# Optimization experiments

Measured on AMD Instinct MI355X. Metric: run time of the kernel, lower is better.

Reference implementation:

```python
import jax, jax.numpy as jnp
import numpy as np

N_NODES = 100000
N_EDGES = 3200000
D_FEAT = 512


def setup_inputs() -> dict:
    key = jax.random.key(0)
    k1, k2, k3, k4 = jax.random.split(key, 4)
    x = jax.random.normal(k1, (N_NODES, D_FEAT), dtype=jnp.float32)
    edge_index = jax.random.randint(k2, (2, N_EDGES), 0, N_NODES, dtype=jnp.int64)
    # Glorot-ish init for GCN layer weights
    W1 = jax.random.normal(k3, (D_FEAT, 16), dtype=jnp.float32) * (1.0 / np.sqrt(D_FEAT))
    b1 = jnp.zeros((16,), dtype=jnp.float32)
    W2 = jax.random.normal(k4, (16, 2), dtype=jnp.float32) * (1.0 / np.sqrt(16))
    b2 = jnp.zeros((2,), dtype=jnp.float32)
    return {"x": x, "edge_index": edge_index, "W1": W1, "b1": b1, "W2": W2, "b2": b2}


def _gcn_prep(edge_index, n_nodes):
    # add self-loops and compute symmetric normalization (GCNConv default)
    row = jnp.concatenate([edge_index[0], jnp.arange(n_nodes, dtype=edge_index.dtype)])
    col = jnp.concatenate([edge_index[1], jnp.arange(n_nodes, dtype=edge_index.dtype)])
    deg = jax.ops.segment_sum(jnp.ones_like(row, dtype=jnp.float32), row,
                              num_segments=n_nodes)
    deg_isqrt = jnp.where(deg > 0, jax.lax.rsqrt(deg), 0.0)
    norm = deg_isqrt[row] * deg_isqrt[col]  # [E+N]
    return row, col, norm


def _gcn_conv(x, W, b, row, col, norm, n_nodes):
    h = x @ W                              # [N, out]
    msg = h[col] * norm[:, None]           # gather + scale  [E+N, out]
    out = jax.ops.segment_sum(msg, row, num_segments=n_nodes)  # scatter-add
    return out + b


def reference(x, edge_index, W1, b1, W2, b2):
    n_nodes = x.shape[0]
    row, col, norm = _gcn_prep(edge_index, n_nodes)
    h = _gcn_conv(x, W1, b1, row, col, norm, n_nodes)
    h = jax.nn.relu(h)
    # dropout is identity in eval mode (deterministic reference)
    h = _gcn_conv(h, W2, b2, row, col, norm, n_nodes)
    return jax.nn.log_softmax(h, axis=1)
```

## Files before the change

### kernel.cpp

```cpp
#include <hip/hip_runtime.h>
#include <math.h>


#define DF 512
#define H1F 16
#define BROWS 256
#define PA_VPT 16
#define PA_BATCH 4096
#define A2_CAP 10240

typedef short bf16x8 __attribute__((ext_vector_type(8)));
typedef float f32x4 __attribute__((ext_vector_type(4)));
typedef _Float16 half8 __attribute__((ext_vector_type(8)));

static __device__ __forceinline__ short bf16_rne(float f) {
    unsigned int u = __builtin_bit_cast(unsigned int, f);
    unsigned int r = (u + 0x7FFFu + ((u >> 16) & 1u)) >> 16;
    return (short)r;
}

__global__ __launch_bounds__(256) void k_hist(const int* __restrict__ rowi,
                                              unsigned int* __restrict__ ghist,
                                              int E, int nbkt, int nblkp) {
    __shared__ unsigned int hist[512];
    int t = threadIdx.x;
    hist[t] = 0u; hist[t + 256] = 0u;
    __syncthreads();
    int base = blockIdx.x * PA_BATCH;
    int ne = E - base; if (ne > PA_BATCH) ne = PA_BATCH;
    for (int j = t; j < ne; j += 256)
        atomicAdd(&hist[(unsigned int)rowi[base + j] >> 8], 1u);
    __syncthreads();
    for (int b = t; b < nbkt; b += 256)
        ghist[(size_t)b * nblkp + blockIdx.x] = hist[b];
}

__global__ __launch_bounds__(256) void k_colscan(const unsigned int* __restrict__ ghist,
                                                 unsigned int* __restrict__ gbase,
                                                 unsigned int* __restrict__ btot,
                                                 int nblk, int nblkp) {
    __shared__ unsigned int s[256];
    int t = threadIdx.x, b = blockIdx.x;
    unsigned int carry = 0u;
    int nch = (nblk + 255) / 256;
    for (int ch = 0; ch < nch; ++ch) {
        int idx = ch * 256 + t;
        unsigned int v = (idx < nblk) ? ghist[(size_t)b * nblkp + idx] : 0u;
        s[t] = v;
        __syncthreads();
        for (int off = 1; off < 256; off <<= 1) {
            unsigned int u = (t >= off) ? s[t - off] : 0u;
            __syncthreads();
            s[t] += u;
            __syncthreads();
        }
        if (idx < nblk) gbase[(size_t)b * nblkp + idx] = carry + s[t] - v;
        unsigned int tot = s[255];
        __syncthreads();
        carry += tot;
    }
    if (t == 0) btot[b] = carry;
}

__global__ __launch_bounds__(256) void k_scatter(const int* __restrict__ rowi,
                                                 const int* __restrict__ coli,
                                                 const unsigned int* __restrict__ gbase,
                                                 const unsigned int* __restrict__ btot,
                                                 unsigned int* __restrict__ pairs,
                                                 int E, int nbkt, int nblkp) {
    __shared__ unsigned int hist[512];
    __shared__ unsigned int sA[512];
    __shared__ unsigned int sB[512];
    __shared__ unsigned int gb[512];
    __shared__ unsigned int reorder[PA_BATCH];
    __shared__ unsigned short bid[PA_BATCH];
    int t = threadIdx.x;
    int base = blockIdx.x * PA_BATCH;
    int ne = E - base; if (ne > PA_BATCH) ne = PA_BATCH;

    unsigned int b0 = (t < nbkt) ? btot[t] : 0u;
    unsigned int b1v = (t + 256 < nbkt) ? btot[t + 256] : 0u;
    sA[t] = b0; sA[t + 256] = b1v;
    __syncthreads();
    {
        unsigned int* src = sA; unsigned int* dst = sB;
        for (int off = 1; off < 512; off <<= 1) {
            unsigned int v0 = src[t] + ((t >= off) ? src[t - off] : 0u);
            unsigned int v1 = src[t + 256] + src[t + 256 - off];
            dst[t] = v0; dst[t + 256] = v1;
            __syncthreads();
            unsigned int* tmp = src; src = dst; dst = tmp;
        }
        gb[t] = src[t] - b0;
        gb[t + 256] = src[t + 256] - b1v;
        if (t < nbkt) gb[t] += gbase[(size_t)t * nblkp + blockIdx.x];
        if (t + 256 < nbkt) gb[t + 256] += gbase[(size_t)(t + 256) * nblkp + blockIdx.x];
    }

    hist[t] = 0u; hist[t + 256] = 0u;
    __syncthreads();

    unsigned int pk[PA_VPT]; unsigned int bk[PA_VPT]; unsigned int rk[PA_VPT];
#pragma unroll
    for (int j = 0; j < PA_VPT; ++j) {
        int idx = j * 256 + t;
        if (idx < ne) {
            int r = rowi[base + idx];
            int c = coli[base + idx];
            unsigned int b = (unsigned int)r >> 8;
            pk[j] = ((unsigned int)(r & (BROWS - 1)) << 17) | (unsigned int)c;
            bk[j] = b;
            rk[j] = atomicAdd(&hist[b], 1u);
        } else bk[j] = 0xFFFFFFFFu;
    }
    __syncthreads();

    sA[t] = hist[t]; sA[t + 256] = hist[t + 256];
    __syncthreads();
    unsigned int* src = sA; unsigned int* dst = sB;
    for (int off = 1; off < 512; off <<= 1) {
        unsigned int v0 = src[t] + ((t >= off) ? src[t - off] : 0u);
        unsigned int v1 = src[t + 256] + src[t + 256 - off];
        dst[t] = v0; dst[t + 256] = v1;
        __syncthreads();
        unsigned int* tmp = src; src = dst; dst = tmp;
    }

#pragma unroll
    for (int j = 0; j < PA_VPT; ++j) {
        if (bk[j] != 0xFFFFFFFFu) {
            unsigned int b = bk[j];
            unsigned int slot = src[b] - hist[b] + rk[j];
            reorder[slot] = pk[j];
            bid[slot] = (unsigned short)b;
        }
    }
    __syncthreads();

    for (int s = t; s < ne; s += 256) {
        unsigned int b = bid[s];
        unsigned int off = src[b] - hist[b];
        pairs[gb[b] + ((unsigned int)s - off)] = reorder[s];
    }
}

__global__ __launch_bounds__(512) void k_count(const unsigned int* __restrict__ pairs,
                                               const unsigned int* __restrict__ btot,
                                               unsigned int* __restrict__ bpref_g,
                                               unsigned int* __restrict__ deg,
                                               unsigned int* __restrict__ rowloc,
                                               float* __restrict__ isq, int n, int nbkt) {
    __shared__ unsigned int bsc[512];
    __shared__ unsigned int rcnt[256];
    __shared__ unsigned int ssc[256];
    int t = threadIdx.x;
    int b = blockIdx.x;
    int r0 = b * 256;

    bsc[t] = (t < nbkt) ? btot[t] : 0u;
    __syncthreads();
    for (int off = 1; off < 512; off <<= 1) {
        unsigned int u = (t >= off) ? bsc[t - off] : 0u;
        __syncthreads();
        bsc[t] += u;
        __syncthreads();
    }
    unsigned int bp = (b > 0) ? bsc[b - 1] : 0u;
    unsigned int cnt = btot[b];
    if (t == 0) bpref_g[b] = bp;
    if (cnt > A2_CAP) cnt = A2_CAP;

    if (t < 256) rcnt[t] = 0u;
    __syncthreads();
    for (unsigned int i = t; i < cnt; i += 512)
        atomicAdd(&rcnt[pairs[bp + i] >> 17], 1u);
    __syncthreads();
    unsigned int d = 0;
    if (t < 256) { d = rcnt[t]; ssc[t] = d; }
    __syncthreads();
    for (int off = 1; off < 256; off <<= 1) {
        unsigned int u = 0;
        if (t < 256 && t >= off) u = ssc[t - off];
        __syncthreads();
        if (t < 256) ssc[t] += u;
        __syncthreads();
    }
    if (t < 256 && r0 + t < n) {
        deg[r0 + t] = d;
        rowloc[r0 + t] = ssc[t] - d;
        isq[r0 + t] = rsqrtf((float)(d + 1u));
    }
}

__global__ __launch_bounds__(256) void k_gemm1(const float* __restrict__ x,
                                               const float* __restrict__ W1,
                                               const float* __restrict__ isq,
                                               _Float16* __restrict__ h1h,
                                               int n, int ntile, int tstride) {
    int wave = threadIdx.x >> 6;
    int lane = threadIdx.x & 63;
    int g = lane >> 4;
    int m = lane & 15;

    bf16x8 wf[16];
#pragma unroll
    for (int s = 0; s < 16; ++s) {
#pragma unroll
        for (int j = 0; j < 8; ++j) {
            int k = s * 32 + g * 8 + j;
            wf[s][j] = bf16_rne(W1[k * H1F + m]);
        }
    }

    for (int tile = blockIdx.x * 4 + wave; tile < ntile; tile += tstride) {
        long r0 = (long)tile * 16;
        const float* xrow = x + (r0 + m) * DF;
        f32x4 acc = {0.0f, 0.0f, 0.0f, 0.0f};
#pragma unroll
        for (int s = 0; s < 16; ++s) {
            const float4* p = (const float4*)(xrow + s * 32 + g * 8);
            float4 a0 = p[0];
            float4 a1 = p[1];
            bf16x8 af;
            af[0] = bf16_rne(a0.x); af[1] = bf16_rne(a0.y);
            af[2] = bf16_rne(a0.z); af[3] = bf16_rne(a0.w);
            af[4] = bf16_rne(a1.x); af[5] = bf16_rne(a1.y);
            af[6] = bf16_rne(a1.z); af[7] = bf16_rne(a1.w);
            acc = __builtin_amdgcn_mfma_f32_16x16x32_bf16(af, wf[s], acc, 0, 0, 0);
        }
#pragma unroll
        for (int j = 0; j < 4; ++j) {
            long rr = r0 + g * 4 + j;
            h1h[rr * H1F + m] = (_Float16)(isq[rr] * acc[j]);
        }
    }
}

__global__ __launch_bounds__(1024) void k_sortg1(unsigned int* __restrict__ pairs,
                                                 const unsigned int* __restrict__ btot,
                                                 const unsigned int* __restrict__ bpref_g,
                                                 const unsigned int* __restrict__ rowloc,
                                                 const float* __restrict__ isq,
                                                 const _Float16* __restrict__ h1h,
                                                 const float* __restrict__ b1,
                                                 _Float16* __restrict__ r1h, int n) {
    __shared__ unsigned int sorted[A2_CAP];
    __shared__ unsigned int rloc[256];
    __shared__ unsigned int rcur[256];
    int t = threadIdx.x;
    int b = blockIdx.x;
    int r0 = b * 256;
    unsigned int bp = bpref_g[b];
    unsigned int cnt = btot[b];
    if (cnt > A2_CAP) cnt = A2_CAP;

    if (t < 256) {
        rloc[t] = (r0 + t < n) ? rowloc[r0 + t] : 0u;
        rcur[t] = 0u;
    }
    __syncthreads();
    for (unsigned int i = t; i < cnt; i += 1024) {
        unsigned int p = pairs[bp + i];
        unsigned int lr = p >> 17;
        unsigned int rk = atomicAdd(&rcur[lr], 1u);
        sorted[rloc[lr] + rk] = p & 0x1FFFFu;
    }
    __syncthreads();
    for (unsigned int i = t; i < cnt; i += 1024) pairs[bp + i] = sorted[i];

    int lr = t >> 2;
    int r = r0 + lr;
    if (r >= n) return;
    int hf = t & 1, sg = (t >> 1) & 1;
    unsigned int start = rloc[lr];
    unsigned int cntr = rcur[lr];
    float s = isq[r];
    const half8* hb = (const half8*)h1h;
    float acc[8];
    if (sg == 0) {
        half8 me = hb[(size_t)r * 2 + hf];
#pragma unroll
        for (int i = 0; i < 8; ++i) acc[i] = (float)me[i];
    } else {
#pragma unroll
        for (int i = 0; i < 8; ++i) acc[i] = 0.0f;
    }
    unsigned int k = sg;
    for (; k + 2 < cntr; k += 4) {
        unsigned int c0 = sorted[start + k];
        unsigned int c1 = sorted[start + k + 2];
        half8 v0 = hb[(size_t)c0 * 2 + hf];
        half8 v1 = hb[(size_t)c1 * 2 + hf];
#pragma unroll
        for (int i = 0; i < 8; ++i) acc[i] += (float)v0[i] + (float)v1[i];
    }
    for (; k < cntr; k += 2) {
        unsigned int c0 = sorted[start + k];
        half8 v0 = hb[(size_t)c0 * 2 + hf];
#pragma unroll
        for (int i = 0; i < 8; ++i) acc[i] += (float)v0[i];
    }
#pragma unroll
    for (int i = 0; i < 8; ++i) acc[i] += __shfl_xor(acc[i], 2);
    if (sg == 0) {
        const float* b1p = b1 + hf * 8;
        half8 o;
#pragma unroll
        for (int i = 0; i < 8; ++i)
            o[i] = (_Float16)(s * fmaxf(fmaf(s, acc[i], b1p[i]), 0.0f));
        ((half8*)r1h)[(size_t)r * 2 + hf] = o;
    }
}

__global__ __launch_bounds__(256) void k_gather2(const _Float16* __restrict__ r1h,
                                                 const unsigned int* __restrict__ deg,
                                                 const unsigned int* __restrict__ bpref,
                                                 const unsigned int* __restrict__ rowloc,
                                                 const unsigned int* __restrict__ csr,
                                                 const float* __restrict__ isq,
                                                 const float* __restrict__ W2,
                                                 const float* __restrict__ b2,
                                                 float* __restrict__ out, int n) {
    int tid = blockIdx.x * 256 + threadIdx.x;
    int r = tid >> 2;
    if (r >= n) return;
    int hf = tid & 1, sg = (tid >> 1) & 1;
    unsigned int start = bpref[(unsigned int)r >> 8] + rowloc[r];
    unsigned int cnt = deg[r];
    float s = isq[r];
    const half8* hb = (const half8*)r1h;
    float acc[8];
    if (sg == 0) {
        half8 me = hb[(size_t)r * 2 + hf];
#pragma unroll
        for (int i = 0; i < 8; ++i) acc[i] = (float)me[i];
    } else {
#pragma unroll
        for (int i = 0; i < 8; ++i) acc[i] = 0.0f;
    }
    unsigned int k = sg;
    for (; k + 2 < cnt; k += 4) {
        unsigned int c0 = csr[start + k];
        unsigned int c1 = csr[start + k + 2];
        half8 v0 = hb[(size_t)c0 * 2 + hf];
        half8 v1 = hb[(size_t)c1 * 2 + hf];
#pragma unroll
        for (int i = 0; i < 8; ++i) acc[i] += (float)v0[i] + (float)v1[i];
    }
    for (; k < cnt; k += 2) {
        unsigned int c0 = csr[start + k];
        half8 v0 = hb[(size_t)c0 * 2 + hf];
#pragma unroll
        for (int i = 0; i < 8; ++i) acc[i] += (float)v0[i];
    }
#pragma unroll
    for (int i = 0; i < 8; ++i) acc[i] += __shfl_xor(acc[i], 2);
    int f0 = hf * 8;
    float o0 = 0.0f, o1 = 0.0f;
#pragma unroll
    for (int i = 0; i < 8; ++i) {
        o0 = fmaf(acc[i], W2[(f0 + i) * 2 + 0], o0);
        o1 = fmaf(acc[i], W2[(f0 + i) * 2 + 1], o1);
    }
    o0 += __shfl_xor(o0, 1);
    o1 += __shfl_xor(o1, 1);
    if ((tid & 3) == 0) {
        float a = fmaf(s, o0, b2[0]);
        float b = fmaf(s, o1, b2[1]);
        float m = fmaxf(a, b);
        float lse = m + logf(expf(a - m) + expf(b - m));
        out[(size_t)r * 2 + 0] = a - lse;
        out[(size_t)r * 2 + 1] = b - lse;
    }
}

extern "C" void kernel_launch(void* const* d_in, const int* in_sizes, int n_in,
                              void* d_out, int out_size, void* d_ws, size_t ws_size,
                              hipStream_t stream) {
    const float* x  = (const float*)d_in[0];
    const int*   ei = (const int*)d_in[1];
    const float* W1 = (const float*)d_in[2];
    const float* b1 = (const float*)d_in[3];
    const float* W2 = (const float*)d_in[4];
    const float* b2 = (const float*)d_in[5];

    int n = in_sizes[0] / DF;
    int E = in_sizes[1] / 2;
    const int* rowi = ei;
    const int* coli = ei + E;

    int NBKT = (n + BROWS - 1) / BROWS;
    int NBLK = (E + PA_BATCH - 1) / PA_BATCH;
    int NBLKP = NBLK + 2;

    char* base = (char*)d_ws;
    unsigned int* deg    = (unsigned int*)base; base += (size_t)n * 4;
    float*        isq    = (float*)base;        base += (size_t)n * 4;
    unsigned int* rowloc = (unsigned int*)base; base += (size_t)n * 4;
    unsigned int* btot   = (unsigned int*)base; base += 512 * 4;
    unsigned int* bpref  = (unsigned int*)base; base += 512 * 4;
    unsigned int* ghist  = (unsigned int*)base; base += (size_t)NBKT * NBLKP * 4;
    unsigned int* gbase  = (unsigned int*)base; base += (size_t)NBKT * NBLKP * 4;
    _Float16*     h1h    = (_Float16*)base;     base += (size_t)n * H1F * 2;
    _Float16*     r1h    = (_Float16*)base;     base += (size_t)n * H1F * 2;
    unsigned int* pairs  = (unsigned int*)base; base += (size_t)E * 4;
    float*        out    = (float*)d_out;

    k_hist<<<NBLK, 256, 0, stream>>>(rowi, ghist, E, NBKT, NBLKP);
    k_colscan<<<NBKT, 256, 0, stream>>>(ghist, gbase, btot, NBLK, NBLKP);
    k_scatter<<<NBLK, 256, 0, stream>>>(rowi, coli, gbase, btot, pairs, E, NBKT, NBLKP);
    k_count<<<NBKT, 512, 0, stream>>>(pairs, btot, bpref, deg, rowloc, isq, n, NBKT);
    {
        int ntile = (n + 15) / 16;
        int ngrid = 782;
        k_gemm1<<<ngrid, 256, 0, stream>>>(x, W1, isq, h1h, n, ntile, ngrid * 4);
    }
    k_sortg1<<<NBKT, 1024, 0, stream>>>(pairs, btot, bpref, rowloc, isq, h1h, b1, r1h, n);
    {
        int work = n * 4;
        k_gather2<<<(work + 255) / 256, 256, 0, stream>>>(r1h, deg, bpref, rowloc, pairs, isq, W2, b2, out, n);
    }
}
```

Baseline: 145.1 us.

## Re-sort buckets in layer-2 kernel instead of writing sorted CSR back; vectorize histogram

The sorted neighbor list is no longer written back to global memory in k_sortg1. Instead k_sortg2 reloads the bucketed pairs and re-sorts them in shared memory before its gather, which also removes the deg array. The histogram kernel now reads row indices with int4 loads for full batches. This trades a global write, a later global read and the deg traffic for a duplicated shared-memory sort. Layer 2 also moves from small 256-thread blocks to 1024-thread blocks with large shared memory, which may reduce occupancy.

```diff
diff --git a/kernel.cpp b/kernel.cpp
--- a/kernel.cpp
+++ b/kernel.cpp
@@ -28,8 +28,20 @@
     __syncthreads();
     int base = blockIdx.x * PA_BATCH;
     int ne = E - base; if (ne > PA_BATCH) ne = PA_BATCH;
-    for (int j = t; j < ne; j += 256)
-        atomicAdd(&hist[(unsigned int)rowi[base + j] >> 8], 1u);
+    if (ne == PA_BATCH) {
+        const int4* p4 = (const int4*)(rowi + base);
+#pragma unroll
+        for (int j = 0; j < 4; ++j) {
+            int4 v = p4[j * 256 + t];
+            atomicAdd(&hist[(unsigned int)v.x >> 8], 1u);
+            atomicAdd(&hist[(unsigned int)v.y >> 8], 1u);
+            atomicAdd(&hist[(unsigned int)v.z >> 8], 1u);
+            atomicAdd(&hist[(unsigned int)v.w >> 8], 1u);
+        }
+    } else {
+        for (int j = t; j < ne; j += 256)
+            atomicAdd(&hist[(unsigned int)rowi[base + j] >> 8], 1u);
+    }
     __syncthreads();
     for (int b = t; b < nbkt; b += 256)
         ghist[(size_t)b * nblkp + blockIdx.x] = hist[b];
@@ -147,7 +159,6 @@
 __global__ __launch_bounds__(512) void k_count(const unsigned int* __restrict__ pairs,
                                                const unsigned int* __restrict__ btot,
                                                unsigned int* __restrict__ bpref_g,
-                                               unsigned int* __restrict__ deg,
                                                unsigned int* __restrict__ rowloc,
                                                float* __restrict__ isq, int n, int nbkt) {
     __shared__ unsigned int bsc[512];
@@ -186,7 +197,6 @@
         __syncthreads();
     }
     if (t < 256 && r0 + t < n) {
-        deg[r0 + t] = d;
         rowloc[r0 + t] = ssc[t] - d;
         isq[r0 + t] = rsqrtf((float)(d + 1u));
     }
@@ -236,7 +246,7 @@
     }
 }
 
-__global__ __launch_bounds__(1024) void k_sortg1(unsigned int* __restrict__ pairs,
+__global__ __launch_bounds__(1024) void k_sortg1(const unsigned int* __restrict__ pairs,
                                                  const unsigned int* __restrict__ btot,
                                                  const unsigned int* __restrict__ bpref_g,
                                                  const unsigned int* __restrict__ rowloc,
@@ -266,7 +276,6 @@
         sorted[rloc[lr] + rk] = p & 0x1FFFFu;
     }
     __syncthreads();
-    for (unsigned int i = t; i < cnt; i += 1024) pairs[bp + i] = sorted[i];
 
     int lr = t >> 2;
     int r = r0 + lr;
@@ -312,21 +321,44 @@
     }
 }
 
-__global__ __launch_bounds__(256) void k_gather2(const _Float16* __restrict__ r1h,
-                                                 const unsigned int* __restrict__ deg,
-                                                 const unsigned int* __restrict__ bpref,
+__global__ __launch_bounds__(1024) void k_sortg2(const unsigned int* __restrict__ pairs,
+                                                 const unsigned int* __restrict__ btot,
+                                                 const unsigned int* __restrict__ bpref_g,
                                                  const unsigned int* __restrict__ rowloc,
-                                                 const unsigned int* __restrict__ csr,
                                                  const float* __restrict__ isq,
+                                                 const _Float16* __restrict__ r1h,
                                                  const float* __restrict__ W2,
                                                  const float* __restrict__ b2,
                                                  float* __restrict__ out, int n) {
-    int tid = blockIdx.x * 256 + threadIdx.x;
-    int r = tid >> 2;
+    __shared__ unsigned int sorted[A2_CAP];
+    __shared__ unsigned int rloc[256];
+    __shared__ unsigned int rcur[256];
+    int t = threadIdx.x;
+    int b = blockIdx.x;
+    int r0 = b * 256;
+    unsigned int bp = bpref_g[b];
+    unsigned int cnt = btot[b];
+    if (cnt > A2_CAP) cnt = A2_CAP;
+
+    if (t < 256) {
+        rloc[t] = (r0 + t < n) ? rowloc[r0 + t] : 0u;
+        rcur[t] = 0u;
+    }
+    __syncthreads();
+    for (unsigned int i = t; i < cnt; i += 1024) {
+        unsigned int p = pairs[bp + i];
+        unsigned int lr = p >> 17;
+        unsigned int rk = atomicAdd(&rcur[lr], 1u);
+        sorted[rloc[lr] + rk] = p & 0x1FFFFu;
+    }
+    __syncthreads();
+
+    int lr = t >> 2;
+    int r = r0 + lr;
     if (r >= n) return;
-    int hf = tid & 1, sg = (tid >> 1) & 1;
-    unsigned int start = bpref[(unsigned int)r >> 8] + rowloc[r];
-    unsigned int cnt = deg[r];
+    int hf = t & 1, sg = (t >> 1) & 1;
+    unsigned int start = rloc[lr];
+    unsigned int cntr = rcur[lr];
     float s = isq[r];
     const half8* hb = (const half8*)r1h;
     float acc[8];
@@ -339,16 +371,16 @@
         for (int i = 0; i < 8; ++i) acc[i] = 0.0f;
     }
     unsigned int k = sg;
-    for (; k + 2 < cnt; k += 4) {
-        unsigned int c0 = csr[start + k];
-        unsigned int c1 = csr[start + k + 2];
+    for (; k + 2 < cntr; k += 4) {
+        unsigned int c0 = sorted[start + k];
+        unsigned int c1 = sorted[start + k + 2];
         half8 v0 = hb[(size_t)c0 * 2 + hf];
         half8 v1 = hb[(size_t)c1 * 2 + hf];
 #pragma unroll
         for (int i = 0; i < 8; ++i) acc[i] += (float)v0[i] + (float)v1[i];
     }
-    for (; k < cnt; k += 2) {
-        unsigned int c0 = csr[start + k];
+    for (; k < cntr; k += 2) {
+        unsigned int c0 = sorted[start + k];
         half8 v0 = hb[(size_t)c0 * 2 + hf];
 #pragma unroll
         for (int i = 0; i < 8; ++i) acc[i] += (float)v0[i];
@@ -364,13 +396,13 @@
     }
     o0 += __shfl_xor(o0, 1);
     o1 += __shfl_xor(o1, 1);
-    if ((tid & 3) == 0) {
+    if ((t & 3) == 0) {
         float a = fmaf(s, o0, b2[0]);
-        float b = fmaf(s, o1, b2[1]);
-        float m = fmaxf(a, b);
-        float lse = m + logf(expf(a - m) + expf(b - m));
+        float bb = fmaf(s, o1, b2[1]);
+        float m = fmaxf(a, bb);
+        float lse = m + logf(expf(a - m) + expf(bb - m));
         out[(size_t)r * 2 + 0] = a - lse;
-        out[(size_t)r * 2 + 1] = b - lse;
+        out[(size_t)r * 2 + 1] = bb - lse;
     }
 }
 
@@ -394,7 +426,6 @@
     int NBLKP = NBLK + 2;
 
     char* base = (char*)d_ws;
-    unsigned int* deg    = (unsigned int*)base; base += (size_t)n * 4;
     float*        isq    = (float*)base;        base += (size_t)n * 4;
     unsigned int* rowloc = (unsigned int*)base; base += (size_t)n * 4;
     unsigned int* btot   = (unsigned int*)base; base += 512 * 4;
@@ -409,15 +440,12 @@
     k_hist<<<NBLK, 256, 0, stream>>>(rowi, ghist, E, NBKT, NBLKP);
     k_colscan<<<NBKT, 256, 0, stream>>>(ghist, gbase, btot, NBLK, NBLKP);
     k_scatter<<<NBLK, 256, 0, stream>>>(rowi, coli, gbase, btot, pairs, E, NBKT, NBLKP);
-    k_count<<<NBKT, 512, 0, stream>>>(pairs, btot, bpref, deg, rowloc, isq, n, NBKT);
+    k_count<<<NBKT, 512, 0, stream>>>(pairs, btot, bpref, rowloc, isq, n, NBKT);
     {
         int ntile = (n + 15) / 16;
         int ngrid = 782;
         k_gemm1<<<ngrid, 256, 0, stream>>>(x, W1, isq, h1h, n, ntile, ngrid * 4);
     }
     k_sortg1<<<NBKT, 1024, 0, stream>>>(pairs, btot, bpref, rowloc, isq, h1h, b1, r1h, n);
-    {
-        int work = n * 4;
-        k_gather2<<<(work + 255) / 256, 256, 0, stream>>>(r1h, deg, bpref, rowloc, pairs, isq, W2, b2, out, n);
-    }
-}
+    k_sortg2<<<NBKT, 1024, 0, stream>>>(pairs, btot, bpref, rowloc, isq, r1h, W2, b2, out, n);
+}
```

New measurement: 130.6 us. -10.0%, faster.
